# Optimization experiments

Hardware: AMD Instinct MI355X
Metric: run time of the kernel (lower is better)

## Reference

```python
import jax, jax.numpy as jnp
import numpy as np

D_MODEL = 1024
D_FEATURE = 64
N_HEADS = D_MODEL // D_FEATURE  # 16


def setup_inputs() -> dict:
    key = jax.random.key(0)
    ks = jax.random.split(key, 11)
    B, S = 2, 2048
    s = 1.0 / np.sqrt(D_MODEL)
    inp = {
        "queries": jax.random.normal(ks[0], (B, S, D_MODEL), dtype=jnp.float32),
        "keys": jax.random.normal(ks[1], (B, S, D_MODEL), dtype=jnp.float32),
        "values": jax.random.normal(ks[2], (B, S, D_MODEL), dtype=jnp.float32),
        # Per-head Q/K/V projection weights stacked over heads: [H, d_model, d_feature]
        "Wq": jax.random.normal(ks[3], (N_HEADS, D_MODEL, D_FEATURE), dtype=jnp.float32) * s,
        "Wk": jax.random.normal(ks[4], (N_HEADS, D_MODEL, D_FEATURE), dtype=jnp.float32) * s,
        "Wv": jax.random.normal(ks[5], (N_HEADS, D_MODEL, D_FEATURE), dtype=jnp.float32) * s,
        "bq": jax.random.normal(ks[6], (N_HEADS, D_FEATURE), dtype=jnp.float32) * 0.01,
        "bk": jax.random.normal(ks[7], (N_HEADS, D_FEATURE), dtype=jnp.float32) * 0.01,
        "bv": jax.random.normal(ks[8], (N_HEADS, D_FEATURE), dtype=jnp.float32) * 0.01,
        # Output projection Linear(d_model, d_model)
        "Wo": jax.random.normal(ks[9], (D_MODEL, D_MODEL), dtype=jnp.float32) * s,
        "bo": jax.random.normal(ks[10], (D_MODEL,), dtype=jnp.float32) * 0.01,
    }
    return inp


def reference(queries, keys, values, Wq, Wk, Wv, bq, bk, bv, Wo, bo):
    # Batched equivalent of the per-head loop: all heads' Q/K/V projections
    # done as single einsums, fused multi-head scaled-dot-product attention,
    # then concat (reshape) + output projection. Dropout is identity (eval).
    scale = 1.0 / jnp.sqrt(jnp.asarray(D_FEATURE, queries.dtype))
    q = jnp.einsum("bsd,hdf->bhsf", queries, Wq) + bq[None, :, None, :]
    k = jnp.einsum("bsd,hdf->bhsf", keys, Wk) + bk[None, :, None, :]
    v = jnp.einsum("bsd,hdf->bhsf", values, Wv) + bv[None, :, None, :]
    scores = jnp.einsum("bhsf,bhtf->bhst", q, k) * scale  # [B,H,S,S]
    attn = jax.nn.softmax(scores, axis=-1)
    out = jnp.einsum("bhst,bhtf->bhsf", attn, v)  # [B,H,S,F]
    B, H, S, F = out.shape
    # torch.cat(heads, dim=2): head outputs laid out contiguously -> (h f)
    out = out.transpose(0, 2, 1, 3).reshape(B, S, H * F)
    return out @ Wo.T + bo  # final Linear(d_model, d_model)
```

## Files before the change

kernel.cpp:

```cpp
#include <hip/hip_runtime.h>
#include <hip/hip_bf16.h>

typedef __bf16 bf16_t;
typedef __bf16 bf16x4 __attribute__((ext_vector_type(4)));
typedef __bf16 bf16x8 __attribute__((ext_vector_type(8)));
typedef _Float16 f16_t;
typedef _Float16 f16x4 __attribute__((ext_vector_type(4)));
typedef _Float16 f16x8 __attribute__((ext_vector_type(8)));
typedef __fp16 hf2 __attribute__((ext_vector_type(2)));
typedef float f32x4 __attribute__((ext_vector_type(4)));

#define MFMA16(a, b, c)  __builtin_amdgcn_mfma_f32_16x16x32_bf16((a), (b), (c), 0, 0, 0)
#define MFMA32H(a, b, c) __builtin_amdgcn_mfma_f32_16x16x32_f16((a), (b), (c), 0, 0, 0)

#define QSCALE 0.18033688089869237f

typedef __attribute__((address_space(3))) void lds_void;
typedef const __attribute__((address_space(1))) void glob_void;
static __device__ __forceinline__ void gl_lds16(const void* g, void* l) {
    __builtin_amdgcn_global_load_lds((glob_void*)g, (lds_void*)l, 16, 0, 0);
}

__global__ __launch_bounds__(256) void prep(
    const float* __restrict__ Wq, const float* __restrict__ Wk,
    const float* __restrict__ Wv, const float* __restrict__ Wo,
    const float* __restrict__ qin, const float* __restrict__ kin,
    const float* __restrict__ vin,
    bf16_t* __restrict__ WqT, bf16_t* __restrict__ WkT,
    bf16_t* __restrict__ WvT, bf16_t* __restrict__ WoT,
    bf16_t* __restrict__ qb, bf16_t* __restrict__ kb, bf16_t* __restrict__ vb)
{
    const int t = threadIdx.x;
    if (blockIdx.x < 256) {
        __shared__ float tile[64][65];
        const int h = blockIdx.x >> 4, d0 = (blockIdx.x & 15) << 6;
        const float* Ws[3] = {Wq, Wk, Wv};
        bf16_t* Wt[3] = {WqT, WkT, WvT};
        const int r = t >> 4, c4 = (t & 15) << 2;
        for (int s = 0; s < 3; ++s) {
            const float* W = Ws[s] + ((size_t)h << 16);
#pragma unroll
            for (int i = 0; i < 4; ++i) {
                float4 v = *(const float4*)&W[(size_t)(d0 + i * 16 + r) * 64 + c4];
                tile[i * 16 + r][c4 + 0] = v.x; tile[i * 16 + r][c4 + 1] = v.y;
                tile[i * 16 + r][c4 + 2] = v.z; tile[i * 16 + r][c4 + 3] = v.w;
            }
            __syncthreads();
#pragma unroll
            for (int i = 0; i < 4; ++i) {
                int f = i * 16 + r;
                bf16x4 o;
                o[0] = (bf16_t)tile[c4 + 0][f]; o[1] = (bf16_t)tile[c4 + 1][f];
                o[2] = (bf16_t)tile[c4 + 2][f]; o[3] = (bf16_t)tile[c4 + 3][f];
                *(bf16x4*)&Wt[s][(((size_t)(h << 6) + f) << 10) + d0 + c4] = o;
            }
            __syncthreads();
        }
    } else {
        size_t id = (size_t)(blockIdx.x - 256) * 256 + t;
        size_t e = id * 4;
        {
            float4 v = *(const float4*)&qin[e];
            bf16x4 o = {(bf16_t)v.x, (bf16_t)v.y, (bf16_t)v.z, (bf16_t)v.w};
            *(bf16x4*)&qb[e] = o;
        }
        {
            float4 v = *(const float4*)&kin[e];
            bf16x4 o = {(bf16_t)v.x, (bf16_t)v.y, (bf16_t)v.z, (bf16_t)v.w};
            *(bf16x4*)&kb[e] = o;
        }
        {
            float4 v = *(const float4*)&vin[e];
            bf16x4 o = {(bf16_t)v.x, (bf16_t)v.y, (bf16_t)v.z, (bf16_t)v.w};
            *(bf16x4*)&vb[e] = o;
        }
        if (id < 262144) {
            float4 v = *(const float4*)&Wo[e];
            bf16x4 o = {(bf16_t)v.x, (bf16_t)v.y, (bf16_t)v.z, (bf16_t)v.w};
            *(bf16x4*)&WoT[e] = o;
        }
    }
}

static __device__ __forceinline__ void gemm_k1024(
    const bf16_t* __restrict__ A, const bf16_t* __restrict__ B,
    int m0, int n0, bf16_t* As, bf16_t* Bs, f32x4 acc[4][4])
{
    const int tid = threadIdx.x, lane = tid & 63, w = tid >> 6;
    const int m = lane & 15, quad = lane >> 4;
    const int wm = (w >> 1) * 64, wn = (w & 1) * 64;
    const int lrow = lane >> 3, lcol = (lane & 7) * 8;

    for (int kt = 0; kt < 1024; kt += 64) {
#pragma unroll
        for (int i = 0; i < 4; ++i) {
            int chunk = i * 4 + w;
            int row = chunk * 8 + lrow;
            gl_lds16(A + (size_t)(m0 + row) * 1024 + kt + lcol, As + chunk * 512);
            gl_lds16(B + (size_t)(n0 + row) * 1024 + kt + lcol, Bs + chunk * 512);
        }
        __syncthreads();
#pragma unroll
        for (int kc = 0; kc < 2; ++kc) {
            bf16x8 af[4], bfr[4];
#pragma unroll
            for (int x = 0; x < 4; ++x) {
                af[x]  = *(const bf16x8*)&As[(wm + x * 16 + m) * 64 + kc * 32 + quad * 8];
                bfr[x] = *(const bf16x8*)&Bs[(wn + x * 16 + m) * 64 + kc * 32 + quad * 8];
            }
#pragma unroll
            for (int mt = 0; mt < 4; ++mt)
#pragma unroll
                for (int nt = 0; nt < 4; ++nt)
                    acc[mt][nt] = MFMA16(af[mt], bfr[nt], acc[mt][nt]);
        }
        __syncthreads();
    }
}

__global__ __launch_bounds__(256) void gemm_proj(
    const bf16_t* __restrict__ qb, const bf16_t* __restrict__ kb,
    const bf16_t* __restrict__ vb, const bf16_t* __restrict__ WT,
    const float* __restrict__ bq, const float* __restrict__ bk,
    const float* __restrict__ bv,
    bf16_t* __restrict__ Qs, bf16_t* __restrict__ Ksb, f16_t* __restrict__ Vt)
{
    __shared__ alignas(16) bf16_t As[8192], Bs[8192];
    const int z = blockIdx.z;
    const bf16_t* A = (z == 0) ? qb : (z == 1) ? kb : vb;
    const bf16_t* B = WT + (size_t)z * (1024 * 1024);
    const float* bias = (z == 0) ? bq : (z == 1) ? bk : bv;
    const int m0 = blockIdx.y * 128, n0 = blockIdx.x * 128;

    f32x4 zero = {0.f, 0.f, 0.f, 0.f};
    f32x4 acc[4][4];
#pragma unroll
    for (int i = 0; i < 4; ++i)
#pragma unroll
        for (int j = 0; j < 4; ++j) acc[i][j] = zero;

    gemm_k1024(A, B, m0, n0, As, Bs, acc);

    const int lane = threadIdx.x & 63, w = threadIdx.x >> 6;
    const int m = lane & 15, quad = lane >> 4;
    const int wm = (w >> 1) * 64, wn = (w & 1) * 64;

    if (z == 2) {
#pragma unroll
        for (int mt = 0; mt < 4; ++mt)
#pragma unroll
            for (int nt = 0; nt < 4; ++nt) {
                int col = n0 + wn + nt * 16 + m;
                float bb = bias[col];
                int row0 = m0 + wm + mt * 16 + quad * 4;
                int bi = row0 >> 11, s = row0 & 2047;
                f16x4 p;
#pragma unroll
                for (int r = 0; r < 4; ++r) p[r] = (f16_t)(acc[mt][nt][r] + bb);
                *(f16x4*)&Vt[((size_t)bi * 1024 + col) * 2048 + s] = p;
            }
    } else {
        bf16_t* out = z ? Ksb : Qs;
        float sc = z ? 1.0f : QSCALE;
#pragma unroll
        for (int mt = 0; mt < 4; ++mt)
#pragma unroll
            for (int nt = 0; nt < 4; ++nt) {
                int col = n0 + wn + nt * 16 + m;
                float bb = bias[col];
#pragma unroll
                for (int r = 0; r < 4; ++r) {
                    int row = m0 + wm + mt * 16 + quad * 4 + r;
                    out[(size_t)row * 1024 + col] = (bf16_t)((acc[mt][nt][r] + bb) * sc);
                }
            }
    }
}

__global__ __launch_bounds__(256) void gemm_out(
    const bf16_t* __restrict__ Aos, const bf16_t* __restrict__ WoT,
    const float* __restrict__ bo, float* __restrict__ out)
{
    __shared__ alignas(16) bf16_t As[128 * 64], Bs[64 * 64];
    const int tid = threadIdx.x, lane = tid & 63, w = tid >> 6;
    const int m = lane & 15, quad = lane >> 4;
    const int wm = (w >> 1) * 64, wn = (w & 1) * 32;
    const int m0 = blockIdx.y * 128, n0 = blockIdx.x * 64;
    const int lrow = lane >> 3, lcol = (lane & 7) * 8;

    f32x4 zero = {0.f, 0.f, 0.f, 0.f};
    f32x4 acc[4][2];
#pragma unroll
    for (int i = 0; i < 4; ++i) { acc[i][0] = zero; acc[i][1] = zero; }

    for (int kt = 0; kt < 1024; kt += 64) {
#pragma unroll
        for (int i = 0; i < 4; ++i) {
            int chunk = i * 4 + w;
            gl_lds16(Aos + (size_t)(m0 + chunk * 8 + lrow) * 1024 + kt + lcol, As + chunk * 512);
        }
#pragma unroll
        for (int i = 0; i < 2; ++i) {
            int chunk = i * 4 + w;
            gl_lds16(WoT + (size_t)(n0 + chunk * 8 + lrow) * 1024 + kt + lcol, Bs + chunk * 512);
        }
        __syncthreads();
#pragma unroll
        for (int kc = 0; kc < 2; ++kc) {
            bf16x8 af[4], bfr[2];
#pragma unroll
            for (int x = 0; x < 4; ++x)
                af[x] = *(const bf16x8*)&As[(wm + x * 16 + m) * 64 + kc * 32 + quad * 8];
#pragma unroll
            for (int x = 0; x < 2; ++x)
                bfr[x] = *(const bf16x8*)&Bs[(wn + x * 16 + m) * 64 + kc * 32 + quad * 8];
#pragma unroll
            for (int mt = 0; mt < 4; ++mt)
#pragma unroll
                for (int nt = 0; nt < 2; ++nt)
                    acc[mt][nt] = MFMA16(af[mt], bfr[nt], acc[mt][nt]);
        }
        __syncthreads();
    }

#pragma unroll
    for (int mt = 0; mt < 4; ++mt)
#pragma unroll
        for (int nt = 0; nt < 2; ++nt) {
            int col = n0 + wn + nt * 16 + m;
            float bb = bo[col];
#pragma unroll
            for (int r = 0; r < 4; ++r) {
                int row = m0 + wm + mt * 16 + quad * 4 + r;
                out[(size_t)row * 1024 + col] = acc[mt][nt][r] + bb;
            }
        }
}

__global__ __launch_bounds__(256, 4) void attn5(
    const bf16_t* __restrict__ Qb, const bf16_t* __restrict__ Kb,
    const f16_t* __restrict__ Vt, f16_t* __restrict__ Op, float* __restrict__ Ls)
{
    __shared__ alignas(16) bf16_t Ks[2][32][72];
    __shared__ alignas(16) f16_t  Vts[2][64][40];

    const int tid = threadIdx.x, lane = tid & 63, w = tid >> 6;
    const int m = lane & 15, quad = lane >> 4;
    const int bh = blockIdx.x, b = bh >> 4, h = bh & 15;
    const int q0 = blockIdx.y * 128;
    const int ks = blockIdx.z;
    const int kt0 = ks << 10;
    const size_t base = (size_t)b * 2048 * 1024 + h * 64;
    const size_t vbase = ((size_t)b * 1024 + h * 64) * 2048;

    bf16x8 aq[2][2];
#pragma unroll
    for (int qt = 0; qt < 2; ++qt) {
        const bf16_t* qp = Qb + base + (size_t)(q0 + w * 32 + qt * 16 + m) * 1024;
        aq[qt][0] = *(const bf16x8*)(qp + quad * 8);
        aq[qt][1] = *(const bf16x8*)(qp + 32 + quad * 8);
    }
    f16x8 ones8;
#pragma unroll
    for (int j = 0; j < 8; ++j) ones8[j] = (f16_t)1.0f;

    f32x4 zero = {0.f, 0.f, 0.f, 0.f};
    f32x4 acc[2][5];
#pragma unroll
    for (int qt = 0; qt < 2; ++qt)
#pragma unroll
        for (int i = 0; i < 5; ++i) acc[qt][i] = zero;

    const int kkey = tid >> 3, kfo = (tid & 7) * 8;
    const int vf = tid >> 2, vko = (tid & 3) * 8;

    bf16x8 rk = *(const bf16x8*)(Kb + base + (size_t)(kt0 + kkey) * 1024 + kfo);
    f16x8  rv = *(const f16x8*)(Vt + vbase + (size_t)vf * 2048 + kt0 + vko);

    int buf = 0;
    for (int kt = kt0; kt < kt0 + 1024; kt += 32) {
        *(bf16x8*)&Ks[buf][kkey][kfo] = rk;
        *(f16x8*)&Vts[buf][vf][vko] = rv;
        __syncthreads();
        if (kt + 32 < kt0 + 1024) {
            rk = *(const bf16x8*)(Kb + base + (size_t)(kt + 32 + kkey) * 1024 + kfo);
            rv = *(const f16x8*)(Vt + vbase + (size_t)vf * 2048 + kt + 32 + vko);
        }

        f32x4 s[2][2];
#pragma unroll
        for (int kl = 0; kl < 2; ++kl) {
            bf16x8 a0 = *(const bf16x8*)&Ks[buf][kl * 16 + m][quad * 8];
            bf16x8 a1 = *(const bf16x8*)&Ks[buf][kl * 16 + m][32 + quad * 8];
#pragma unroll
            for (int qt = 0; qt < 2; ++qt) {
                f32x4 t = MFMA16(a0, aq[qt][0], zero);
                s[kl][qt] = MFMA16(a1, aq[qt][1], t);
            }
        }

        f16x8 p[2];
#pragma unroll
        for (int qt = 0; qt < 2; ++qt)
#pragma unroll
            for (int kl = 0; kl < 2; ++kl) {
                hf2 lo = __builtin_amdgcn_cvt_pkrtz(
                    __builtin_amdgcn_exp2f(s[kl][qt][0]),
                    __builtin_amdgcn_exp2f(s[kl][qt][1]));
                hf2 hi = __builtin_amdgcn_cvt_pkrtz(
                    __builtin_amdgcn_exp2f(s[kl][qt][2]),
                    __builtin_amdgcn_exp2f(s[kl][qt][3]));
                p[qt][kl * 4 + 0] = lo[0]; p[qt][kl * 4 + 1] = lo[1];
                p[qt][kl * 4 + 2] = hi[0]; p[qt][kl * 4 + 3] = hi[1];
            }

#pragma unroll
        for (int ft = 0; ft < 4; ++ft) {
            f16x4 lo = *(const f16x4*)&Vts[buf][ft * 16 + m][quad * 4];
            f16x4 hi = *(const f16x4*)&Vts[buf][ft * 16 + m][16 + quad * 4];
            f16x8 bv;
#pragma unroll
            for (int j = 0; j < 4; ++j) { bv[j] = lo[j]; bv[4 + j] = hi[j]; }
#pragma unroll
            for (int qt = 0; qt < 2; ++qt)
                acc[qt][ft] = MFMA32H(p[qt], bv, acc[qt][ft]);
        }
#pragma unroll
        for (int qt = 0; qt < 2; ++qt)
            acc[qt][4] = MFMA32H(p[qt], ones8, acc[qt][4]);

        buf ^= 1;
    }

#pragma unroll
    for (int qt = 0; qt < 2; ++qt)
#pragma unroll
        for (int r = 0; r < 4; ++r) {
            int grow = (b << 11) + q0 + w * 32 + qt * 16 + quad * 4 + r;
            f16_t* op = Op + (((size_t)ks << 12) + grow) * 1024 + (h << 6);
#pragma unroll
            for (int ft = 0; ft < 4; ++ft)
                op[ft * 16 + m] = (f16_t)(acc[qt][ft][r]);
            if (m == 0)
                Ls[((((size_t)ks << 12) + grow) << 4) + h] = acc[qt][4][r];
        }
}

__global__ __launch_bounds__(256) void combine(
    const f16_t* __restrict__ Op, const float* __restrict__ Ls,
    bf16_t* __restrict__ Os)
{
    size_t idx = ((size_t)blockIdx.x * 256 + threadIdx.x) * 8;
    int row = (int)(idx >> 10), h = (int)((idx & 1023) >> 6);
    f16x8 a = *(const f16x8*)&Op[idx];
    f16x8 c = *(const f16x8*)&Op[(size_t)4096 * 1024 + idx];
    float l = Ls[row * 16 + h] + Ls[4096 * 16 + row * 16 + h];
    float inv = __builtin_amdgcn_rcpf(l);
    bf16x8 o;
#pragma unroll
    for (int i = 0; i < 8; ++i)
        o[i] = (bf16_t)(((float)a[i] + (float)c[i]) * inv);
    *(bf16x8*)&Os[idx] = o;
}

extern "C" void kernel_launch(void* const* d_in, const int* in_sizes, int n_in,
                              void* d_out, int out_size, void* d_ws, size_t ws_size,
                              hipStream_t stream)
{
    const float* queries = (const float*)d_in[0];
    const float* keys    = (const float*)d_in[1];
    const float* values  = (const float*)d_in[2];
    const float* Wq = (const float*)d_in[3];
    const float* Wk = (const float*)d_in[4];
    const float* Wv = (const float*)d_in[5];
    const float* bq = (const float*)d_in[6];
    const float* bk = (const float*)d_in[7];
    const float* bv = (const float*)d_in[8];
    const float* Wo = (const float*)d_in[9];
    const float* bo = (const float*)d_in[10];

    char* ws = (char*)d_ws;
    const size_t MB = 1024 * 1024;
    bf16_t* WqT = (bf16_t*)(ws + 0 * MB);
    bf16_t* WkT = (bf16_t*)(ws + 2 * MB);
    bf16_t* WvT = (bf16_t*)(ws + 4 * MB);
    bf16_t* WoT = (bf16_t*)(ws + 6 * MB);
    bf16_t* qb  = (bf16_t*)(ws + 8 * MB);
    bf16_t* kb  = (bf16_t*)(ws + 16 * MB);
    bf16_t* vb  = (bf16_t*)(ws + 24 * MB);
    f16_t*  Vt  = (f16_t*)(ws + 32 * MB);
    f16_t*  Op  = (f16_t*)(ws + 40 * MB);
    float*  Lsp = (float*)(ws + 56 * MB);
    bf16_t* Qs  = (bf16_t*)d_out;
    bf16_t* Ksb = (bf16_t*)((char*)d_out + 8 * MB);
    bf16_t* Os  = qb;
    (void)WkT; (void)WvT;

    prep<<<4352, 256, 0, stream>>>(Wq, Wk, Wv, Wo, queries, keys, values,
                                   WqT, WkT, WvT, WoT, qb, kb, vb);

    gemm_proj<<<dim3(8, 32, 3), 256, 0, stream>>>(qb, kb, vb, WqT, bq, bk, bv,
                                                  Qs, Ksb, Vt);

    attn5<<<dim3(32, 16, 2), 256, 0, stream>>>(Qs, Ksb, Vt, Op, Lsp);

    combine<<<2048, 256, 0, stream>>>(Op, Lsp, Os);

    gemm_out<<<dim3(16, 32), 256, 0, stream>>>(Os, WoT, bo, (float*)d_out);
}
```

Before: 234.1 us.

## Shrink projection GEMM tile to 128x64 and XOR-swizzle LDS layout

Projection GEMM tiles shrink from 128x128 to 128x64, which doubles the grid to 1536 blocks. The kernel also gets a launch-bounds occupancy hint of 6. Both projection and output GEMMs now share one core routine that XOR-swizzles the LDS column chunk by row, to avoid bank conflicts on the bf16x8 fragment reads. Smaller tiles lower per-block reuse of the A operand but raise occupancy and load balance across CUs.

```diff
diff --git a/kernel.cpp b/kernel.cpp
--- a/kernel.cpp
+++ b/kernel.cpp
@@ -82,74 +82,81 @@
     }
 }
 
-static __device__ __forceinline__ void gemm_k1024(
+static __device__ __forceinline__ void gemm_core(
     const bf16_t* __restrict__ A, const bf16_t* __restrict__ B,
-    int m0, int n0, bf16_t* As, bf16_t* Bs, f32x4 acc[4][4])
+    int m0, int n0, int K, bf16_t* As, bf16_t* Bs, f32x4 acc[4][2])
 {
     const int tid = threadIdx.x, lane = tid & 63, w = tid >> 6;
     const int m = lane & 15, quad = lane >> 4;
-    const int wm = (w >> 1) * 64, wn = (w & 1) * 64;
-    const int lrow = lane >> 3, lcol = (lane & 7) * 8;
-
-    for (int kt = 0; kt < 1024; kt += 64) {
+    const int wm = (w >> 1) * 64, wn = (w & 1) * 32;
+    const int lrow = lane >> 3;
+    const int lcol = (((lane & 7) ^ (lrow & 7)) << 3);
+
+    for (int kt = 0; kt < K; kt += 64) {
 #pragma unroll
         for (int i = 0; i < 4; ++i) {
             int chunk = i * 4 + w;
-            int row = chunk * 8 + lrow;
-            gl_lds16(A + (size_t)(m0 + row) * 1024 + kt + lcol, As + chunk * 512);
-            gl_lds16(B + (size_t)(n0 + row) * 1024 + kt + lcol, Bs + chunk * 512);
+            gl_lds16(A + (size_t)(m0 + chunk * 8 + lrow) * K + kt + lcol, As + chunk * 512);
+        }
+#pragma unroll
+        for (int i = 0; i < 2; ++i) {
+            int chunk = i * 4 + w;
+            gl_lds16(B + (size_t)(n0 + chunk * 8 + lrow) * K + kt + lcol, Bs + chunk * 512);
         }
         __syncthreads();
 #pragma unroll
         for (int kc = 0; kc < 2; ++kc) {
-            bf16x8 af[4], bfr[4];
+            bf16x8 af[4], bfr[2];
 #pragma unroll
             for (int x = 0; x < 4; ++x) {
-                af[x]  = *(const bf16x8*)&As[(wm + x * 16 + m) * 64 + kc * 32 + quad * 8];
-                bfr[x] = *(const bf16x8*)&Bs[(wn + x * 16 + m) * 64 + kc * 32 + quad * 8];
+                int row = wm + x * 16 + m;
+                af[x] = *(const bf16x8*)&As[row * 64 + (((kc * 4 + quad) ^ (m & 7)) << 3)];
+            }
+#pragma unroll
+            for (int x = 0; x < 2; ++x) {
+                int row = wn + x * 16 + m;
+                bfr[x] = *(const bf16x8*)&Bs[row * 64 + (((kc * 4 + quad) ^ (m & 7)) << 3)];
             }
 #pragma unroll
             for (int mt = 0; mt < 4; ++mt)
 #pragma unroll
-                for (int nt = 0; nt < 4; ++nt)
+                for (int nt = 0; nt < 2; ++nt)
                     acc[mt][nt] = MFMA16(af[mt], bfr[nt], acc[mt][nt]);
         }
         __syncthreads();
     }
 }
 
-__global__ __launch_bounds__(256) void gemm_proj(
+__global__ __launch_bounds__(256, 6) void gemm_proj(
     const bf16_t* __restrict__ qb, const bf16_t* __restrict__ kb,
     const bf16_t* __restrict__ vb, const bf16_t* __restrict__ WT,
     const float* __restrict__ bq, const float* __restrict__ bk,
     const float* __restrict__ bv,
     bf16_t* __restrict__ Qs, bf16_t* __restrict__ Ksb, f16_t* __restrict__ Vt)
 {
-    __shared__ alignas(16) bf16_t As[8192], Bs[8192];
+    __shared__ alignas(16) bf16_t As[128 * 64], Bs[64 * 64];
     const int z = blockIdx.z;
     const bf16_t* A = (z == 0) ? qb : (z == 1) ? kb : vb;
     const bf16_t* B = WT + (size_t)z * (1024 * 1024);
     const float* bias = (z == 0) ? bq : (z == 1) ? bk : bv;
-    const int m0 = blockIdx.y * 128, n0 = blockIdx.x * 128;
+    const int m0 = blockIdx.y * 128, n0 = blockIdx.x * 64;
 
     f32x4 zero = {0.f, 0.f, 0.f, 0.f};
-    f32x4 acc[4][4];
-#pragma unroll
-    for (int i = 0; i < 4; ++i)
-#pragma unroll
-        for (int j = 0; j < 4; ++j) acc[i][j] = zero;
-
-    gemm_k1024(A, B, m0, n0, As, Bs, acc);
+    f32x4 acc[4][2];
+#pragma unroll
+    for (int i = 0; i < 4; ++i) { acc[i][0] = zero; acc[i][1] = zero; }
+
+    gemm_core(A, B, m0, n0, 1024, As, Bs, acc);
 
     const int lane = threadIdx.x & 63, w = threadIdx.x >> 6;
     const int m = lane & 15, quad = lane >> 4;
-    const int wm = (w >> 1) * 64, wn = (w & 1) * 64;
+    const int wm = (w >> 1) * 64, wn = (w & 1) * 32;
 
     if (z == 2) {
 #pragma unroll
         for (int mt = 0; mt < 4; ++mt)
 #pragma unroll
-            for (int nt = 0; nt < 4; ++nt) {
+            for (int nt = 0; nt < 2; ++nt) {
                 int col = n0 + wn + nt * 16 + m;
                 float bb = bias[col];
                 int row0 = m0 + wm + mt * 16 + quad * 4;
@@ -165,7 +172,7 @@
 #pragma unroll
         for (int mt = 0; mt < 4; ++mt)
 #pragma unroll
-            for (int nt = 0; nt < 4; ++nt) {
+            for (int nt = 0; nt < 2; ++nt) {
                 int col = n0 + wn + nt * 16 + m;
                 float bb = bias[col];
 #pragma unroll
@@ -182,47 +189,18 @@
     const float* __restrict__ bo, float* __restrict__ out)
 {
     __shared__ alignas(16) bf16_t As[128 * 64], Bs[64 * 64];
-    const int tid = threadIdx.x, lane = tid & 63, w = tid >> 6;
+    const int m0 = blockIdx.y * 128, n0 = blockIdx.x * 64;
+
+    f32x4 zero = {0.f, 0.f, 0.f, 0.f};
+    f32x4 acc[4][2];
+#pragma unroll
+    for (int i = 0; i < 4; ++i) { acc[i][0] = zero; acc[i][1] = zero; }
+
+    gemm_core(Aos, WoT, m0, n0, 1024, As, Bs, acc);
+
+    const int lane = threadIdx.x & 63, w = threadIdx.x >> 6;
     const int m = lane & 15, quad = lane >> 4;
     const int wm = (w >> 1) * 64, wn = (w & 1) * 32;
-    const int m0 = blockIdx.y * 128, n0 = blockIdx.x * 64;
-    const int lrow = lane >> 3, lcol = (lane & 7) * 8;
-
-    f32x4 zero = {0.f, 0.f, 0.f, 0.f};
-    f32x4 acc[4][2];
-#pragma unroll
-    for (int i = 0; i < 4; ++i) { acc[i][0] = zero; acc[i][1] = zero; }
-
-    for (int kt = 0; kt < 1024; kt += 64) {
-#pragma unroll
-        for (int i = 0; i < 4; ++i) {
-            int chunk = i * 4 + w;
-            gl_lds16(Aos + (size_t)(m0 + chunk * 8 + lrow) * 1024 + kt + lcol, As + chunk * 512);
-        }
-#pragma unroll
-        for (int i = 0; i < 2; ++i) {
-            int chunk = i * 4 + w;
-            gl_lds16(WoT + (size_t)(n0 + chunk * 8 + lrow) * 1024 + kt + lcol, Bs + chunk * 512);
-        }
-        __syncthreads();
-#pragma unroll
-        for (int kc = 0; kc < 2; ++kc) {
-            bf16x8 af[4], bfr[2];
-#pragma unroll
-            for (int x = 0; x < 4; ++x)
-                af[x] = *(const bf16x8*)&As[(wm + x * 16 + m) * 64 + kc * 32 + quad * 8];
-#pragma unroll
-            for (int x = 0; x < 2; ++x)
-                bfr[x] = *(const bf16x8*)&Bs[(wn + x * 16 + m) * 64 + kc * 32 + quad * 8];
-#pragma unroll
-            for (int mt = 0; mt < 4; ++mt)
-#pragma unroll
-                for (int nt = 0; nt < 2; ++nt)
-                    acc[mt][nt] = MFMA16(af[mt], bfr[nt], acc[mt][nt]);
-        }
-        __syncthreads();
-    }
-
 #pragma unroll
     for (int mt = 0; mt < 4; ++mt)
 #pragma unroll
@@ -399,8 +377,8 @@
     prep<<<4352, 256, 0, stream>>>(Wq, Wk, Wv, Wo, queries, keys, values,
                                    WqT, WkT, WvT, WoT, qb, kb, vb);
 
-    gemm_proj<<<dim3(8, 32, 3), 256, 0, stream>>>(qb, kb, vb, WqT, bq, bk, bv,
-                                                  Qs, Ksb, Vt);
+    gemm_proj<<<dim3(16, 32, 3), 256, 0, stream>>>(qb, kb, vb, WqT, bq, bk, bv,
+                                                   Qs, Ksb, Vt);
 
     attn5<<<dim3(32, 16, 2), 256, 0, stream>>>(Qs, Ksb, Vt, Op, Lsp);
 
```

Result: slower. 241.7 us (+3.3%).
